# Performance work log

Measured on AMD Instinct MI355X. Metric: run time of the kernel, lower is better.

## Reference

```python
import jax, jax.numpy as jnp
import numpy as np

B, L, D, H, N = 1, 768, 128, 8, 6  # batch, seq len, model dim, heads, core_num
DH = D // H
EPS = 1e-5


def _layernorm(x, g, b):
    m = jnp.mean(x, axis=-1, keepdims=True)
    v = jnp.mean(jnp.square(x - m), axis=-1, keepdims=True)
    return (x - m) * jax.lax.rsqrt(v + EPS) * g + b


def setup_inputs() -> dict:
    key = jax.random.key(0)
    ks = jax.random.split(key, 12)
    s = 0.05

    def w(k, shape):
        return jax.random.normal(k, shape, dtype=jnp.float32) * s

    return {
        "x": jax.random.normal(ks[0], (B, L, D), dtype=jnp.float32),
        # JCrossOutProduct: l (in->mid), lo (mid->out); torch Linear convention y = x @ W.T + b
        "cop_l_w": w(ks[1], (N, D, D)), "cop_l_b": jnp.zeros((N, D), jnp.float32),
        "cop_lo_w": w(ks[2], (N, D, D)), "cop_lo_b": jnp.zeros((N, D), jnp.float32),
        # JResCOPAttn.l
        "cop_out_w": w(ks[3], (N, D, D)), "cop_out_b": jnp.zeros((N, D), jnp.float32),
        "cop_ln_g": jnp.ones((N, D), jnp.float32), "cop_ln_b": jnp.zeros((N, D), jnp.float32),
        # nn.MultiheadAttention: packed qkv in_proj + out_proj
        "qkv_w": w(ks[4], (N, 3 * D, D)), "qkv_b": jnp.zeros((N, 3 * D), jnp.float32),
        "mha_out_w": w(ks[5], (N, D, D)), "mha_out_b": jnp.zeros((N, D), jnp.float32),
        "mha_ln_g": jnp.ones((N, D), jnp.float32), "mha_ln_b": jnp.zeros((N, D), jnp.float32),
        # final l1
        "l1_w": w(ks[6], (D, D)), "l1_b": jnp.zeros((D,), jnp.float32),
    }


def reference(x, cop_l_w, cop_l_b, cop_lo_w, cop_lo_b, cop_out_w, cop_out_b,
              cop_ln_g, cop_ln_b, qkv_w, qkv_b, mha_out_w, mha_out_b,
              mha_ln_g, mha_ln_b, l1_w, l1_b):
    scale = 1.0 / np.sqrt(DH)
    for i in range(N):
        # ---- JResCOPAttn branch (AlphaFold-style outer product mean) ----
        a = x @ cop_l_w[i].T + cop_l_b[i]                          # [B,L,D]
        tm = jnp.einsum('bic,bjc->bijc', a, a)                     # [B,L,L,D] outer product
        tm = jnp.einsum('bijc,oc->bijo', tm, cop_lo_w[i]) + cop_lo_b[i]
        tx = x @ cop_out_w[i].T + cop_out_b[i]                     # [B,L,D]
        y1 = x + jnp.einsum('bijo,bjo->bio', tm, tx)               # '...cab,...ab->...cb'
        x1 = _layernorm(y1, cop_ln_g[i], cop_ln_b[i])              # dropout/act are identity
        # ---- JResSelfAttn branch (standard MHA, batch_first) ----
        qkv = x @ qkv_w[i].T + qkv_b[i]                            # [B,L,3D]
        q, k, v = jnp.split(qkv, 3, axis=-1)
        q = q.reshape(B, L, H, DH)
        k = k.reshape(B, L, H, DH)
        v = v.reshape(B, L, H, DH)
        scores = jnp.einsum('bihd,bjhd->bhij', q, k) * scale       # [B,H,L,L]
        attn = jax.nn.softmax(scores, axis=-1)
        o = jnp.einsum('bhij,bjhd->bihd', attn, v).reshape(B, L, D)
        y2 = x + (o @ mha_out_w[i].T + mha_out_b[i])
        x2 = _layernorm(y2, mha_ln_g[i], mha_ln_b[i])
        # ---- combine ----
        x = x + x1 + x2
    return x @ l1_w.T + l1_b
```

## Files before the change

kernel.cpp:

```cpp
#include <hip/hip_runtime.h>

#define L_SEQ 768
#define P_SZ  (L_SEQ * 128)

__device__ __forceinline__ void stage16(int tid, int r0, bool first,
    bool writeback, const float* xprev, const float* y1, const float* y2,
    const float* g1, const float* b1, const float* g2, const float* b2,
    float* xcur, float (*As)[132])
{
    const int row = tid >> 4;
    const int cs  = (tid & 15) * 8;
    const int gr  = (r0 + row) * 128 + cs;
    if (first) {
#pragma unroll
        for (int u = 0; u < 2; ++u)
            *(float4*)&As[row][cs + 4 * u] = *(const float4*)&xprev[gr + 4 * u];
        return;
    }
    float4 v1[2], v2[2];
    float s1 = 0.0f, s2 = 0.0f;
#pragma unroll
    for (int u = 0; u < 2; ++u) {
        v1[u] = *(const float4*)&y1[gr + 4 * u];
        v2[u] = *(const float4*)&y2[gr + 4 * u];
        s1 += v1[u].x + v1[u].y + v1[u].z + v1[u].w;
        s2 += v2[u].x + v2[u].y + v2[u].z + v2[u].w;
    }
#pragma unroll
    for (int m = 1; m < 16; m <<= 1) { s1 += __shfl_xor(s1, m); s2 += __shfl_xor(s2, m); }
    const float mu1 = s1 * (1.0f / 128.0f), mu2 = s2 * (1.0f / 128.0f);
    float q1 = 0.0f, q2 = 0.0f;
#pragma unroll
    for (int u = 0; u < 2; ++u) {
        float d;
        d = v1[u].x - mu1; q1 += d * d;  d = v1[u].y - mu1; q1 += d * d;
        d = v1[u].z - mu1; q1 += d * d;  d = v1[u].w - mu1; q1 += d * d;
        d = v2[u].x - mu2; q2 += d * d;  d = v2[u].y - mu2; q2 += d * d;
        d = v2[u].z - mu2; q2 += d * d;  d = v2[u].w - mu2; q2 += d * d;
    }
#pragma unroll
    for (int m = 1; m < 16; m <<= 1) { q1 += __shfl_xor(q1, m); q2 += __shfl_xor(q2, m); }
    const float rs1 = rsqrtf(q1 * (1.0f / 128.0f) + 1e-5f);
    const float rs2 = rsqrtf(q2 * (1.0f / 128.0f) + 1e-5f);
#pragma unroll
    for (int u = 0; u < 2; ++u) {
        float4 ga = *(const float4*)&g1[cs + 4 * u];
        float4 ba = *(const float4*)&b1[cs + 4 * u];
        float4 gb = *(const float4*)&g2[cs + 4 * u];
        float4 bb = *(const float4*)&b2[cs + 4 * u];
        float4 xv = *(const float4*)&xprev[gr + 4 * u];
        float4 o;
        o.x = xv.x + (v1[u].x - mu1) * rs1 * ga.x + ba.x + (v2[u].x - mu2) * rs2 * gb.x + bb.x;
        o.y = xv.y + (v1[u].y - mu1) * rs1 * ga.y + ba.y + (v2[u].y - mu2) * rs2 * gb.y + bb.y;
        o.z = xv.z + (v1[u].z - mu1) * rs1 * ga.z + ba.z + (v2[u].z - mu2) * rs2 * gb.z + bb.z;
        o.w = xv.w + (v1[u].w - mu1) * rs1 * ga.w + ba.w + (v2[u].w - mu2) * rs2 * gb.w + bb.w;
        *(float4*)&As[row][cs + 4 * u] = o;
        if (writeback) *(float4*)&xcur[gr + 4 * u] = o;
    }
}

__global__ __launch_bounds__(256, 4) void megaK(int first,
    const float* __restrict__ xprev, const float* __restrict__ y1,
    const float* __restrict__ y2, float* __restrict__ xcur,
    const float* __restrict__ g1, const float* __restrict__ b1,
    const float* __restrict__ g2, const float* __restrict__ b2,
    const float* __restrict__ lw, const float* __restrict__ lb,
    const float* __restrict__ ow, const float* __restrict__ ob,
    const float* __restrict__ qw, const float* __restrict__ qb,
    float* __restrict__ a, float* __restrict__ tx, float* __restrict__ qkv)
{
    __shared__ float Bs[64][132];
    __shared__ float As[16][132];
    const int bid = blockIdx.x;
    const int tid = threadIdx.x;
    const int ct = bid / 48, rt = bid % 48;
    const int r0 = rt * 16;
    stage16(tid, r0, first != 0, (!first && ct == 0), xprev, y1, y2,
            g1, b1, g2, b2, xcur, As);
    const float* W; const float* bias; float* outp; int ldC, colbase;
    if (ct < 2)      { W = lw; bias = lb; outp = a;   ldC = 128; colbase = ct * 64; }
    else if (ct < 4) { W = ow; bias = ob; outp = tx;  ldC = 128; colbase = (ct - 2) * 64; }
    else             { W = qw; bias = qb; outp = qkv; ldC = 384; colbase = (ct - 4) * 64; }
#pragma unroll
    for (int t = 0; t < 8; ++t) {
        int idx = tid + 256 * t;
        int brow = idx >> 5, f4 = idx & 31;
        *(float4*)&Bs[brow][f4 * 4] = *(const float4*)&W[(colbase + brow) * 128 + f4 * 4];
    }
    __syncthreads();
    const int rg = tid >> 4, ng = tid & 15;
    float accs[4];
#pragma unroll
    for (int c = 0; c < 4; ++c) accs[c] = bias[colbase + ng + 16 * c];
#pragma unroll 8
    for (int kk = 0; kk < 32; ++kk) {
        float4 a1 = *(const float4*)&As[rg][kk * 4];
#pragma unroll
        for (int c = 0; c < 4; ++c) {
            float4 b = *(const float4*)&Bs[ng + 16 * c][kk * 4];
            accs[c] += a1.x * b.x + a1.y * b.y + a1.z * b.z + a1.w * b.w;
        }
    }
    const int r = r0 + rg;
#pragma unroll
    for (int c = 0; c < 4; ++c)
        outp[r * ldC + colbase + ng + 16 * c] = accs[c];
}

__global__ __launch_bounds__(256, 4) void k2K(const float* __restrict__ qkv,
    const float* __restrict__ a_, const float* __restrict__ tx_,
    float* __restrict__ o_, float* __restrict__ Mpart, float* __restrict__ tspart)
{
    __shared__ __align__(16) char smem[49152];
    const int bid = blockIdx.x;
    const int tid = threadIdx.x;
    if (bid < 384) {
        float* Ks = (float*)smem;
        float* Vs = Ks + 192 * 20;
        float* sm = Vs + 192 * 20;
        float* sl = sm + 256;
        float* sacc = sl + 256;
        const int h = bid / 48;
        const int ch = bid % 48;
        const int r = tid & 15;
        const int part = tid >> 4;
        const int qi = ch * 16 + r;

        float q[16];
        {
            const float4* qr = (const float4*)(qkv + qi * 384 + h * 16);
#pragma unroll
            for (int s = 0; s < 4; ++s) {
                float4 v = qr[s];
                q[s * 4 + 0] = v.x; q[s * 4 + 1] = v.y;
                q[s * 4 + 2] = v.z; q[s * 4 + 3] = v.w;
            }
        }
        float m = -1e30f, l = 0.0f;
        float acc[16];
#pragma unroll
        for (int d = 0; d < 16; ++d) acc[d] = 0.0f;

        for (int s = 0; s < 4; ++s) {
            __syncthreads();
#pragma unroll
            for (int t = 0; t < 3; ++t) {
                int idx = tid + 256 * t;
                int row = idx >> 2, d4 = idx & 3;
                int j = s * 192 + row;
                *(float4*)&Ks[row * 20 + d4 * 4] =
                    *(const float4*)&qkv[j * 384 + 128 + h * 16 + d4 * 4];
                *(float4*)&Vs[row * 20 + d4 * 4] =
                    *(const float4*)&qkv[j * 384 + 256 + h * 16 + d4 * 4];
            }
            __syncthreads();
            const int tb = part * 12;
            for (int jj = 0; jj < 12; ++jj) {
                int t = tb + jj;
                float sc = 0.0f;
#pragma unroll
                for (int d = 0; d < 16; ++d) sc += q[d] * Ks[t * 20 + d];
                sc *= 0.25f;
                if (sc > m + 8.0f) {
                    float f = __expf(m - sc);
                    l *= f;
#pragma unroll
                    for (int d = 0; d < 16; ++d) acc[d] *= f;
                    m = sc;
                }
                float p = __expf(sc - m);
                l += p;
#pragma unroll
                for (int d = 0; d < 16; ++d) acc[d] += p * Vs[t * 20 + d];
            }
        }
        sm[part * 16 + r] = m;
        sl[part * 16 + r] = l;
#pragma unroll
        for (int d = 0; d < 16; ++d) sacc[(part * 16 + r) * 16 + d] = acc[d];
        __syncthreads();

        const int row = tid >> 4, d = tid & 15;
        float M = sm[row];
#pragma unroll
        for (int p = 1; p < 16; ++p) M = fmaxf(M, sm[p * 16 + row]);
        float L = 0.0f, o = 0.0f;
#pragma unroll
        for (int p = 0; p < 16; ++p) {
            float f = __expf(sm[p * 16 + row] - M);
            L += sl[p * 16 + row] * f;
            o += sacc[(p * 16 + row) * 16 + d] * f;
        }
        o_[(ch * 16 + row) * 128 + h * 16 + d] = o / L;
    } else {
        const int idx0 = bid - 384;
        const int jc = idx0 >> 2, ot = idx0 & 3;
        float* As  = (float*)smem;
        float* Ts  = As + 48 * 128;
        float* red = Ts + 48 * 32;
        const int c4 = tid & 31, owt = tid >> 5;
        float accm[4][4] = {};
        float tsacc = 0.0f;
        for (int half = 0; half < 2; ++half) {
            const int j0 = jc * 96 + half * 48;
            __syncthreads();
#pragma unroll
            for (int t = 0; t < 6; ++t) {
                int ix = tid + 256 * t;
                int jj = ix >> 5, f4 = ix & 31;
                *(float4*)&As[jj * 128 + f4 * 4] =
                    *(const float4*)&a_[(j0 + jj) * 128 + f4 * 4];
            }
#pragma unroll
            for (int t = 0; t < 2; ++t) {
                int ix = tid + 256 * t;
                if (ix < 384) {
                    int jj = ix >> 3, f4 = ix & 7;
                    *(float4*)&Ts[jj * 32 + f4 * 4] =
                        *(const float4*)&tx_[(j0 + jj) * 128 + ot * 32 + f4 * 4];
                }
            }
            __syncthreads();
#pragma unroll 4
            for (int jj = 0; jj < 48; ++jj) {
                float4 av = *(const float4*)&As[jj * 128 + c4 * 4];
                float4 tv = *(const float4*)&Ts[jj * 32 + owt * 4];
                float avv[4] = {av.x, av.y, av.z, av.w};
                float tvv[4] = {tv.x, tv.y, tv.z, tv.w};
#pragma unroll
                for (int oi = 0; oi < 4; ++oi)
#pragma unroll
                    for (int ci = 0; ci < 4; ++ci)
                        accm[oi][ci] += avv[ci] * tvv[oi];
            }
            {
                const int o = tid & 31, g = tid >> 5;
                float s = 0.0f;
#pragma unroll
                for (int jj = 0; jj < 6; ++jj) s += Ts[(g * 6 + jj) * 32 + o];
                tsacc += s;
            }
        }
#pragma unroll
        for (int oi = 0; oi < 4; ++oi) {
            *(float4*)&Mpart[jc * 16384 + (ot * 32 + owt * 4 + oi) * 128 + c4 * 4] =
                make_float4(accm[oi][0], accm[oi][1], accm[oi][2], accm[oi][3]);
        }
        __syncthreads();
        {
            const int o = tid & 31, g = tid >> 5;
            red[g * 32 + o] = tsacc;
        }
        __syncthreads();
        if (tid < 32) {
            float s = 0.0f;
#pragma unroll
            for (int g = 0; g < 8; ++g) s += red[g * 32 + tid];
            tspart[jc * 128 + ot * 32 + tid] = s;
        }
    }
}

__global__ __launch_bounds__(256, 4) void ygemmK(
    const float* __restrict__ a_, const float* __restrict__ o_,
    const float* __restrict__ Mpart, const float* __restrict__ lo_w,
    const float* __restrict__ lob, const float* __restrict__ tspart,
    const float* __restrict__ mw, const float* __restrict__ mb,
    const float* __restrict__ xc, float* __restrict__ y1, float* __restrict__ y2)
{
    __shared__ float Bs[64][132];
    const int bid = blockIdx.x;
    const int tid = threadIdx.x;
    const int yb = bid / 48, rt = bid % 48;
    const float* A; float* C; int colbase;
    if (yb < 2) {
        colbase = yb * 64; A = a_; C = y1;
#pragma unroll
        for (int t = 0; t < 8; ++t) {
            int idx = tid + 256 * t;
            int row = idx >> 5, f4 = idx & 31;
            int o = colbase + row;
            float4 s = make_float4(0.f, 0.f, 0.f, 0.f);
#pragma unroll
            for (int jc = 0; jc < 8; ++jc) {
                float4 mv = *(const float4*)&Mpart[jc * 16384 + o * 128 + f4 * 4];
                s.x += mv.x; s.y += mv.y; s.z += mv.z; s.w += mv.w;
            }
            float4 lw4 = *(const float4*)&lo_w[o * 128 + f4 * 4];
            s.x *= lw4.x; s.y *= lw4.y; s.z *= lw4.z; s.w *= lw4.w;
            *(float4*)&Bs[row][f4 * 4] = s;
        }
    } else {
        colbase = (yb - 2) * 64; A = o_; C = y2;
#pragma unroll
        for (int t = 0; t < 8; ++t) {
            int idx = tid + 256 * t;
            int row = idx >> 5, f4 = idx & 31;
            *(float4*)&Bs[row][f4 * 4] =
                *(const float4*)&mw[(colbase + row) * 128 + f4 * 4];
        }
    }
    __syncthreads();
    const int rg = tid >> 4, ng = tid & 15;
    const int r = rt * 16 + rg;
    float accs[4];
#pragma unroll
    for (int c = 0; c < 4; ++c) {
        int gc = colbase + ng + 16 * c;
        float bv;
        if (yb < 2) {
            float s = 0.0f;
#pragma unroll
            for (int jc = 0; jc < 8; ++jc) s += tspart[jc * 128 + gc];
            bv = lob[gc] * s;
        } else {
            bv = mb[gc];
        }
        accs[c] = bv;
    }
    const float* A1 = A + r * 128;
#pragma unroll 8
    for (int kk = 0; kk < 32; ++kk) {
        float4 a1 = *(const float4*)&A1[kk * 4];
#pragma unroll
        for (int c = 0; c < 4; ++c) {
            float4 b = *(const float4*)&Bs[ng + 16 * c][kk * 4];
            accs[c] += a1.x * b.x + a1.y * b.y + a1.z * b.z + a1.w * b.w;
        }
    }
#pragma unroll
    for (int c = 0; c < 4; ++c) {
        int gc = colbase + ng + 16 * c;
        C[r * 128 + gc] = xc[r * 128 + gc] + accs[c];
    }
}

__global__ __launch_bounds__(256, 4) void finK(
    const float* __restrict__ xprev, const float* __restrict__ y1,
    const float* __restrict__ y2,
    const float* __restrict__ g1, const float* __restrict__ b1,
    const float* __restrict__ g2, const float* __restrict__ b2,
    const float* __restrict__ w, const float* __restrict__ bias,
    float* __restrict__ outp)
{
    __shared__ float Bs[64][132];
    __shared__ float As[16][132];
    const int bid = blockIdx.x;
    const int tid = threadIdx.x;
    const int ct = bid / 48, rt = bid % 48;
    const int r0 = rt * 16;
    const int colbase = ct * 64;
    stage16(tid, r0, false, false, xprev, y1, y2, g1, b1, g2, b2, nullptr, As);
#pragma unroll
    for (int t = 0; t < 8; ++t) {
        int idx = tid + 256 * t;
        int brow = idx >> 5, f4 = idx & 31;
        *(float4*)&Bs[brow][f4 * 4] = *(const float4*)&w[(colbase + brow) * 128 + f4 * 4];
    }
    __syncthreads();
    const int rg = tid >> 4, ng = tid & 15;
    float accs[4];
#pragma unroll
    for (int c = 0; c < 4; ++c) accs[c] = bias[colbase + ng + 16 * c];
#pragma unroll 8
    for (int kk = 0; kk < 32; ++kk) {
        float4 a1 = *(const float4*)&As[rg][kk * 4];
#pragma unroll
        for (int c = 0; c < 4; ++c) {
            float4 b = *(const float4*)&Bs[ng + 16 * c][kk * 4];
            accs[c] += a1.x * b.x + a1.y * b.y + a1.z * b.z + a1.w * b.w;
        }
    }
    const int r = r0 + rg;
#pragma unroll
    for (int c = 0; c < 4; ++c)
        outp[r * 128 + colbase + ng + 16 * c] = accs[c];
}

extern "C" void kernel_launch(void* const* d_in, const int* in_sizes, int n_in,
                              void* d_out, int out_size, void* d_ws, size_t ws_size,
                              hipStream_t stream)
{
    const float* x_in      = (const float*)d_in[0];
    const float* cop_l_w   = (const float*)d_in[1];
    const float* cop_l_b   = (const float*)d_in[2];
    const float* cop_lo_w  = (const float*)d_in[3];
    const float* cop_lo_b  = (const float*)d_in[4];
    const float* cop_out_w = (const float*)d_in[5];
    const float* cop_out_b = (const float*)d_in[6];
    const float* cop_ln_g  = (const float*)d_in[7];
    const float* cop_ln_b  = (const float*)d_in[8];
    const float* qkv_w     = (const float*)d_in[9];
    const float* qkv_b     = (const float*)d_in[10];
    const float* mha_out_w = (const float*)d_in[11];
    const float* mha_out_b = (const float*)d_in[12];
    const float* mha_ln_g  = (const float*)d_in[13];
    const float* mha_ln_b  = (const float*)d_in[14];
    const float* l1_w      = (const float*)d_in[15];
    const float* l1_b      = (const float*)d_in[16];

    float* ws = (float*)d_ws;
    float* xA     = ws + 0 * P_SZ;
    float* xB     = ws + 1 * P_SZ;
    float* a_     = ws + 2 * P_SZ;
    float* tx_    = ws + 3 * P_SZ;
    float* y1_    = ws + 4 * P_SZ;
    float* y2_    = ws + 5 * P_SZ;
    float* qkv_   = ws + 6 * P_SZ;
    float* o_     = ws + 9 * P_SZ;
    float* Mpart  = ws + 10 * P_SZ;
    float* tspart = Mpart + 8 * 16384;

    const float* xc = x_in;

    for (int i = 0; i < 6; ++i) {
        const float* lw  = cop_l_w   + i * 16384;
        const float* lb  = cop_l_b   + i * 128;
        const float* low = cop_lo_w  + i * 16384;
        const float* lob = cop_lo_b  + i * 128;
        const float* ow  = cop_out_w + i * 16384;
        const float* ob  = cop_out_b + i * 128;
        const float* qw  = qkv_w     + i * 49152;
        const float* qb  = qkv_b     + i * 384;
        const float* mw  = mha_out_w + i * 16384;
        const float* mb  = mha_out_b + i * 128;
        const float* pg1 = cop_ln_g + (i - 1) * 128;
        const float* pb1 = cop_ln_b + (i - 1) * 128;
        const float* pg2 = mha_ln_g + (i - 1) * 128;
        const float* pb2 = mha_ln_b + (i - 1) * 128;

        if (i == 0) {
            megaK<<<480, 256, 0, stream>>>(1, x_in, nullptr, nullptr, nullptr,
                                           nullptr, nullptr, nullptr, nullptr,
                                           lw, lb, ow, ob, qw, qb, a_, tx_, qkv_);
        } else {
            float* xn = (i & 1) ? xB : xA;
            megaK<<<480, 256, 0, stream>>>(0, xc, y1_, y2_, xn,
                                           pg1, pb1, pg2, pb2,
                                           lw, lb, ow, ob, qw, qb, a_, tx_, qkv_);
            xc = xn;
        }
        k2K<<<416, 256, 0, stream>>>(qkv_, a_, tx_, o_, Mpart, tspart);
        ygemmK<<<192, 256, 0, stream>>>(a_, o_, Mpart, low, lob, tspart, mw, mb,
                                        xc, y1_, y2_);
    }

    finK<<<96, 256, 0, stream>>>(xc, y1_, y2_,
                                 cop_ln_g + 5 * 128, cop_ln_b + 5 * 128,
                                 mha_ln_g + 5 * 128, mha_ln_b + 5 * 128,
                                 l1_w, l1_b, (float*)d_out);
}
```

Baseline: 256.9 us.

## Fuse output projections into attention/COP kernel, drop ygemm kernel

```diff
diff --git a/kernel.cpp b/kernel.cpp
--- a/kernel.cpp
+++ b/kernel.cpp
@@ -67,7 +67,8 @@
     const float* __restrict__ lw, const float* __restrict__ lb,
     const float* __restrict__ ow, const float* __restrict__ ob,
     const float* __restrict__ qw, const float* __restrict__ qb,
-    float* __restrict__ a, float* __restrict__ tx, float* __restrict__ qkv)
+    float* __restrict__ a, float* __restrict__ tx, float* __restrict__ qkv,
+    float* __restrict__ y2i, const float* __restrict__ mbv)
 {
     __shared__ float Bs[64][132];
     __shared__ float As[16][132];
@@ -77,6 +78,18 @@
     const int r0 = rt * 16;
     stage16(tid, r0, first != 0, (!first && ct == 0), xprev, y1, y2,
             g1, b1, g2, b2, xcur, As);
+    if (ct == 0) {
+        const int row = tid >> 4, cs = (tid & 15) * 8;
+        const int gr = (r0 + row) * 128 + cs;
+        float4 m0 = *(const float4*)&mbv[cs];
+        float4 m1 = *(const float4*)&mbv[cs + 4];
+        float4 v0 = *(float4*)&As[row][cs];
+        float4 v1 = *(float4*)&As[row][cs + 4];
+        v0.x += m0.x; v0.y += m0.y; v0.z += m0.z; v0.w += m0.w;
+        v1.x += m1.x; v1.y += m1.y; v1.z += m1.z; v1.w += m1.w;
+        *(float4*)&y2i[gr] = v0;
+        *(float4*)&y2i[gr + 4] = v1;
+    }
     const float* W; const float* bias; float* outp; int ldC, colbase;
     if (ct < 2)      { W = lw; bias = lb; outp = a;   ldC = 128; colbase = ct * 64; }
     else if (ct < 4) { W = ow; bias = ob; outp = tx;  ldC = 128; colbase = (ct - 2) * 64; }
@@ -107,11 +120,13 @@
         outp[r * ldC + colbase + ng + 16 * c] = accs[c];
 }
 
-__global__ __launch_bounds__(256, 4) void k2K(const float* __restrict__ qkv,
+__global__ __launch_bounds__(256) void k2K(const float* __restrict__ qkv,
     const float* __restrict__ a_, const float* __restrict__ tx_,
-    float* __restrict__ o_, float* __restrict__ Mpart, float* __restrict__ tspart)
+    const float* __restrict__ xc, const float* __restrict__ lo_w,
+    const float* __restrict__ lob, const float* __restrict__ mw,
+    float* __restrict__ y1, float* __restrict__ y2)
 {
-    __shared__ __align__(16) char smem[49152];
+    __shared__ __align__(16) char smem[61440];
     const int bid = blockIdx.x;
     const int tid = threadIdx.x;
     if (bid < 384) {
@@ -180,158 +195,113 @@
         for (int d = 0; d < 16; ++d) sacc[(part * 16 + r) * 16 + d] = acc[d];
         __syncthreads();
 
-        const int row = tid >> 4, d = tid & 15;
-        float M = sm[row];
-#pragma unroll
-        for (int p = 1; p < 16; ++p) M = fmaxf(M, sm[p * 16 + row]);
-        float L = 0.0f, o = 0.0f;
-#pragma unroll
-        for (int p = 0; p < 16; ++p) {
-            float f = __expf(sm[p * 16 + row] - M);
-            L += sl[p * 16 + row] * f;
-            o += sacc[(p * 16 + row) * 16 + d] * f;
-        }
-        o_[(ch * 16 + row) * 128 + h * 16 + d] = o / L;
+        float* o16s = (float*)smem;
+        {
+            const int row = tid >> 4, d = tid & 15;
+            float M = sm[row];
+#pragma unroll
+            for (int p = 1; p < 16; ++p) M = fmaxf(M, sm[p * 16 + row]);
+            float L = 0.0f, o = 0.0f;
+#pragma unroll
+            for (int p = 0; p < 16; ++p) {
+                float f = __expf(sm[p * 16 + row] - M);
+                L += sl[p * 16 + row] * f;
+                o += sacc[(p * 16 + row) * 16 + d] * f;
+            }
+            o16s[row * 16 + d] = o / L;
+        }
+        __syncthreads();
+
+        {
+            const int r2 = tid >> 4, cg = tid & 15;
+            float ov[16];
+#pragma unroll
+            for (int s = 0; s < 4; ++s) {
+                float4 t = *(const float4*)&o16s[r2 * 16 + s * 4];
+                ov[s * 4 + 0] = t.x; ov[s * 4 + 1] = t.y;
+                ov[s * 4 + 2] = t.z; ov[s * 4 + 3] = t.w;
+            }
+            const int rg2 = ch * 16 + r2;
+#pragma unroll
+            for (int mm = 0; mm < 8; ++mm) {
+                int mcol = cg * 8 + mm;
+                const float* mwr = &mw[mcol * 128 + h * 16];
+                float s = 0.0f;
+#pragma unroll
+                for (int d2 = 0; d2 < 16; ++d2) s += ov[d2] * mwr[d2];
+                unsafeAtomicAdd(&y2[rg2 * 128 + mcol], s);
+            }
+        }
     } else {
-        const int idx0 = bid - 384;
-        const int jc = idx0 >> 2, ot = idx0 & 3;
+        const int oc0 = (bid - 384) * 8;
         float* As  = (float*)smem;
-        float* Ts  = As + 48 * 128;
-        float* red = Ts + 48 * 32;
-        const int c4 = tid & 31, owt = tid >> 5;
-        float accm[4][4] = {};
-        float tsacc = 0.0f;
-        for (int half = 0; half < 2; ++half) {
-            const int j0 = jc * 96 + half * 48;
-            __syncthreads();
-#pragma unroll
-            for (int t = 0; t < 6; ++t) {
+        float* Ts  = As + 96 * 132;
+        float* W2s = Ts + 96 * 8;
+        float* tss = W2s + 8 * 132;
+        const int c = tid & 127, oq = tid >> 7;
+        float macc[4] = {0.f, 0.f, 0.f, 0.f};
+        float tsl = 0.0f;
+        for (int jc = 0; jc < 8; ++jc) {
+            __syncthreads();
+#pragma unroll
+            for (int t = 0; t < 12; ++t) {
                 int ix = tid + 256 * t;
                 int jj = ix >> 5, f4 = ix & 31;
-                *(float4*)&As[jj * 128 + f4 * 4] =
-                    *(const float4*)&a_[(j0 + jj) * 128 + f4 * 4];
-            }
-#pragma unroll
-            for (int t = 0; t < 2; ++t) {
+                *(float4*)&As[jj * 132 + f4 * 4] =
+                    *(const float4*)&a_[(jc * 96 + jj) * 128 + f4 * 4];
+            }
+            if (tid < 192) {
+                int jj = tid >> 1, qq = tid & 1;
+                *(float4*)&Ts[jj * 8 + qq * 4] =
+                    *(const float4*)&tx_[(jc * 96 + jj) * 128 + oc0 + qq * 4];
+            }
+            __syncthreads();
+#pragma unroll 4
+            for (int jj = 0; jj < 96; ++jj) {
+                float av = As[jj * 132 + c];
+                float4 t4 = *(const float4*)&Ts[jj * 8 + oq * 4];
+                macc[0] += av * t4.x; macc[1] += av * t4.y;
+                macc[2] += av * t4.z; macc[3] += av * t4.w;
+            }
+            if (tid < 8) {
+                float s = 0.0f;
+                for (int jj = 0; jj < 96; ++jj) s += Ts[jj * 8 + tid];
+                tsl += s;
+            }
+        }
+        __syncthreads();
+#pragma unroll
+        for (int k = 0; k < 4; ++k) {
+            int o = oq * 4 + k;
+            W2s[o * 132 + c] = lo_w[(oc0 + o) * 128 + c] * macc[k];
+        }
+        if (tid < 8) tss[tid] = tsl;
+        __syncthreads();
+        for (int jc = 0; jc < 8; ++jc) {
+#pragma unroll
+            for (int t = 0; t < 12; ++t) {
                 int ix = tid + 256 * t;
-                if (ix < 384) {
-                    int jj = ix >> 3, f4 = ix & 7;
-                    *(float4*)&Ts[jj * 32 + f4 * 4] =
-                        *(const float4*)&tx_[(j0 + jj) * 128 + ot * 32 + f4 * 4];
+                int jj = ix >> 5, f4 = ix & 31;
+                *(float4*)&As[jj * 132 + f4 * 4] =
+                    *(const float4*)&a_[(jc * 96 + jj) * 128 + f4 * 4];
+            }
+            __syncthreads();
+#pragma unroll
+            for (int rep = 0; rep < 3; ++rep) {
+                int idx = tid + 256 * rep;
+                int jj = idx >> 3, o = idx & 7;
+                float s = 0.0f;
+#pragma unroll 8
+                for (int c4 = 0; c4 < 32; ++c4) {
+                    float4 av = *(const float4*)&As[jj * 132 + c4 * 4];
+                    float4 wv = *(const float4*)&W2s[o * 132 + c4 * 4];
+                    s += av.x * wv.x + av.y * wv.y + av.z * wv.z + av.w * wv.w;
                 }
-            }
-            __syncthreads();
-#pragma unroll 4
-            for (int jj = 0; jj < 48; ++jj) {
-                float4 av = *(const float4*)&As[jj * 128 + c4 * 4];
-                float4 tv = *(const float4*)&Ts[jj * 32 + owt * 4];
-                float avv[4] = {av.x, av.y, av.z, av.w};
-                float tvv[4] = {tv.x, tv.y, tv.z, tv.w};
-#pragma unroll
-                for (int oi = 0; oi < 4; ++oi)
-#pragma unroll
-                    for (int ci = 0; ci < 4; ++ci)
-                        accm[oi][ci] += avv[ci] * tvv[oi];
-            }
-            {
-                const int o = tid & 31, g = tid >> 5;
-                float s = 0.0f;
-#pragma unroll
-                for (int jj = 0; jj < 6; ++jj) s += Ts[(g * 6 + jj) * 32 + o];
-                tsacc += s;
-            }
-        }
-#pragma unroll
-        for (int oi = 0; oi < 4; ++oi) {
-            *(float4*)&Mpart[jc * 16384 + (ot * 32 + owt * 4 + oi) * 128 + c4 * 4] =
-                make_float4(accm[oi][0], accm[oi][1], accm[oi][2], accm[oi][3]);
-        }
-        __syncthreads();
-        {
-            const int o = tid & 31, g = tid >> 5;
-            red[g * 32 + o] = tsacc;
-        }
-        __syncthreads();
-        if (tid < 32) {
-            float s = 0.0f;
-#pragma unroll
-            for (int g = 0; g < 8; ++g) s += red[g * 32 + tid];
-            tspart[jc * 128 + ot * 32 + tid] = s;
-        }
-    }
-}
-
-__global__ __launch_bounds__(256, 4) void ygemmK(
-    const float* __restrict__ a_, const float* __restrict__ o_,
-    const float* __restrict__ Mpart, const float* __restrict__ lo_w,
-    const float* __restrict__ lob, const float* __restrict__ tspart,
-    const float* __restrict__ mw, const float* __restrict__ mb,
-    const float* __restrict__ xc, float* __restrict__ y1, float* __restrict__ y2)
-{
-    __shared__ float Bs[64][132];
-    const int bid = blockIdx.x;
-    const int tid = threadIdx.x;
-    const int yb = bid / 48, rt = bid % 48;
-    const float* A; float* C; int colbase;
-    if (yb < 2) {
-        colbase = yb * 64; A = a_; C = y1;
-#pragma unroll
-        for (int t = 0; t < 8; ++t) {
-            int idx = tid + 256 * t;
-            int row = idx >> 5, f4 = idx & 31;
-            int o = colbase + row;
-            float4 s = make_float4(0.f, 0.f, 0.f, 0.f);
-#pragma unroll
-            for (int jc = 0; jc < 8; ++jc) {
-                float4 mv = *(const float4*)&Mpart[jc * 16384 + o * 128 + f4 * 4];
-                s.x += mv.x; s.y += mv.y; s.z += mv.z; s.w += mv.w;
-            }
-            float4 lw4 = *(const float4*)&lo_w[o * 128 + f4 * 4];
-            s.x *= lw4.x; s.y *= lw4.y; s.z *= lw4.z; s.w *= lw4.w;
-            *(float4*)&Bs[row][f4 * 4] = s;
-        }
-    } else {
-        colbase = (yb - 2) * 64; A = o_; C = y2;
-#pragma unroll
-        for (int t = 0; t < 8; ++t) {
-            int idx = tid + 256 * t;
-            int row = idx >> 5, f4 = idx & 31;
-            *(float4*)&Bs[row][f4 * 4] =
-                *(const float4*)&mw[(colbase + row) * 128 + f4 * 4];
-        }
-    }
-    __syncthreads();
-    const int rg = tid >> 4, ng = tid & 15;
-    const int r = rt * 16 + rg;
-    float accs[4];
-#pragma unroll
-    for (int c = 0; c < 4; ++c) {
-        int gc = colbase + ng + 16 * c;
-        float bv;
-        if (yb < 2) {
-            float s = 0.0f;
-#pragma unroll
-            for (int jc = 0; jc < 8; ++jc) s += tspart[jc * 128 + gc];
-            bv = lob[gc] * s;
-        } else {
-            bv = mb[gc];
-        }
-        accs[c] = bv;
-    }
-    const float* A1 = A + r * 128;
-#pragma unroll 8
-    for (int kk = 0; kk < 32; ++kk) {
-        float4 a1 = *(const float4*)&A1[kk * 4];
-#pragma unroll
-        for (int c = 0; c < 4; ++c) {
-            float4 b = *(const float4*)&Bs[ng + 16 * c][kk * 4];
-            accs[c] += a1.x * b.x + a1.y * b.y + a1.z * b.z + a1.w * b.w;
-        }
-    }
-#pragma unroll
-    for (int c = 0; c < 4; ++c) {
-        int gc = colbase + ng + 16 * c;
-        C[r * 128 + gc] = xc[r * 128 + gc] + accs[c];
+                int gj = jc * 96 + jj, go = oc0 + o;
+                y1[gj * 128 + go] = xc[gj * 128 + go] + s + lob[go] * tss[o];
+            }
+            __syncthreads();
+        }
     }
 }
 
@@ -400,16 +370,14 @@
     const float* l1_b      = (const float*)d_in[16];
 
     float* ws = (float*)d_ws;
-    float* xA     = ws + 0 * P_SZ;
-    float* xB     = ws + 1 * P_SZ;
-    float* a_     = ws + 2 * P_SZ;
-    float* tx_    = ws + 3 * P_SZ;
-    float* y1_    = ws + 4 * P_SZ;
-    float* y2_    = ws + 5 * P_SZ;
-    float* qkv_   = ws + 6 * P_SZ;
-    float* o_     = ws + 9 * P_SZ;
-    float* Mpart  = ws + 10 * P_SZ;
-    float* tspart = Mpart + 8 * 16384;
+    float* xA   = ws + 0 * P_SZ;
+    float* xB   = ws + 1 * P_SZ;
+    float* a_   = ws + 2 * P_SZ;
+    float* tx_  = ws + 3 * P_SZ;
+    float* y1_  = ws + 4 * P_SZ;
+    float* y2A  = ws + 5 * P_SZ;
+    float* y2B  = ws + 6 * P_SZ;
+    float* qkv_ = ws + 7 * P_SZ;
 
     const float* xc = x_in;
 
@@ -429,23 +397,26 @@
         const float* pg2 = mha_ln_g + (i - 1) * 128;
         const float* pb2 = mha_ln_b + (i - 1) * 128;
 
+        float* y2cur  = (i & 1) ? y2B : y2A;
+        float* y2prev = (i & 1) ? y2A : y2B;
+
         if (i == 0) {
             megaK<<<480, 256, 0, stream>>>(1, x_in, nullptr, nullptr, nullptr,
                                            nullptr, nullptr, nullptr, nullptr,
-                                           lw, lb, ow, ob, qw, qb, a_, tx_, qkv_);
+                                           lw, lb, ow, ob, qw, qb, a_, tx_, qkv_,
+                                           y2cur, mb);
         } else {
             float* xn = (i & 1) ? xB : xA;
-            megaK<<<480, 256, 0, stream>>>(0, xc, y1_, y2_, xn,
+            megaK<<<480, 256, 0, stream>>>(0, xc, y1_, y2prev, xn,
                                            pg1, pb1, pg2, pb2,
-                                           lw, lb, ow, ob, qw, qb, a_, tx_, qkv_);
+                                           lw, lb, ow, ob, qw, qb, a_, tx_, qkv_,
+                                           y2cur, mb);
             xc = xn;
         }
-        k2K<<<416, 256, 0, stream>>>(qkv_, a_, tx_, o_, Mpart, tspart);
-        ygemmK<<<192, 256, 0, stream>>>(a_, o_, Mpart, low, lob, tspart, mw, mb,
-                                        xc, y1_, y2_);
-    }
-
-    finK<<<96, 256, 0, stream>>>(xc, y1_, y2_,
+        k2K<<<400, 256, 0, stream>>>(qkv_, a_, tx_, xc, low, lob, mw, y1_, y2cur);
+    }
+
+    finK<<<96, 256, 0, stream>>>(xc, y1_, y2B,
                                  cop_ln_g + 5 * 128, cop_ln_b + 5 * 128,
                                  mha_ln_g + 5 * 128, mha_ln_b + 5 * 128,
                                  l1_w, l1_b, (float*)d_out);
```

Result: slower. 487.3 us (+89.7%).

## Stage all K rows in LDS once and stream V directly from global memory

Applied to the files above, without the earlier changes.

```diff
diff --git a/kernel.cpp b/kernel.cpp
--- a/kernel.cpp
+++ b/kernel.cpp
@@ -107,19 +107,15 @@
         outp[r * ldC + colbase + ng + 16 * c] = accs[c];
 }
 
-__global__ __launch_bounds__(256, 4) void k2K(const float* __restrict__ qkv,
+__global__ __launch_bounds__(256, 3) void k2K(const float* __restrict__ qkv,
     const float* __restrict__ a_, const float* __restrict__ tx_,
     float* __restrict__ o_, float* __restrict__ Mpart, float* __restrict__ tspart)
 {
-    __shared__ __align__(16) char smem[49152];
+    __shared__ __align__(16) char smem[50176];
     const int bid = blockIdx.x;
     const int tid = threadIdx.x;
     if (bid < 384) {
         float* Ks = (float*)smem;
-        float* Vs = Ks + 192 * 20;
-        float* sm = Vs + 192 * 20;
-        float* sl = sm + 256;
-        float* sacc = sl + 256;
         const int h = bid / 48;
         const int ch = bid % 48;
         const int r = tid & 15;
@@ -136,44 +132,58 @@
                 q[s * 4 + 2] = v.z; q[s * 4 + 3] = v.w;
             }
         }
+#pragma unroll
+        for (int t = 0; t < 12; ++t) {
+            int idx = tid + 256 * t;
+            int row = idx >> 2, seg = idx & 3;
+            *(float4*)&Ks[row * 16 + (row / 48) * 4 + seg * 4] =
+                *(const float4*)&qkv[row * 384 + 128 + h * 16 + seg * 4];
+        }
+        __syncthreads();
+
         float m = -1e30f, l = 0.0f;
         float acc[16];
 #pragma unroll
         for (int d = 0; d < 16; ++d) acc[d] = 0.0f;
 
-        for (int s = 0; s < 4; ++s) {
-            __syncthreads();
-#pragma unroll
-            for (int t = 0; t < 3; ++t) {
-                int idx = tid + 256 * t;
-                int row = idx >> 2, d4 = idx & 3;
-                int j = s * 192 + row;
-                *(float4*)&Ks[row * 20 + d4 * 4] =
-                    *(const float4*)&qkv[j * 384 + 128 + h * 16 + d4 * 4];
-                *(float4*)&Vs[row * 20 + d4 * 4] =
-                    *(const float4*)&qkv[j * 384 + 256 + h * 16 + d4 * 4];
-            }
-            __syncthreads();
-            const int tb = part * 12;
-            for (int jj = 0; jj < 12; ++jj) {
-                int t = tb + jj;
-                float sc = 0.0f;
-#pragma unroll
-                for (int d = 0; d < 16; ++d) sc += q[d] * Ks[t * 20 + d];
-                sc *= 0.25f;
-                if (sc > m + 8.0f) {
-                    float f = __expf(m - sc);
-                    l *= f;
-#pragma unroll
-                    for (int d = 0; d < 16; ++d) acc[d] *= f;
-                    m = sc;
-                }
-                float p = __expf(sc - m);
-                l += p;
-#pragma unroll
-                for (int d = 0; d < 16; ++d) acc[d] += p * Vs[t * 20 + d];
-            }
-        }
+        const int tb = part * 48;
+        const int kb = part * 772;
+        const float* vcol = qkv + 256 + h * 16;
+#pragma unroll 2
+        for (int jj = 0; jj < 48; ++jj) {
+            const float* vr = vcol + (tb + jj) * 384;
+            float4 va = *(const float4*)vr;
+            float4 vb = *(const float4*)(vr + 4);
+            float4 vc = *(const float4*)(vr + 8);
+            float4 vd = *(const float4*)(vr + 12);
+            const float* kr = &Ks[kb + jj * 16];
+            float sc = 0.0f;
+#pragma unroll
+            for (int s = 0; s < 4; ++s) {
+                float4 k4 = *(const float4*)(kr + s * 4);
+                sc += q[s * 4 + 0] * k4.x + q[s * 4 + 1] * k4.y +
+                      q[s * 4 + 2] * k4.z + q[s * 4 + 3] * k4.w;
+            }
+            sc *= 0.25f;
+            if (sc > m + 8.0f) {
+                float f = __expf(m - sc);
+                l *= f;
+#pragma unroll
+                for (int d = 0; d < 16; ++d) acc[d] *= f;
+                m = sc;
+            }
+            float p = __expf(sc - m);
+            l += p;
+            acc[0]  += p * va.x; acc[1]  += p * va.y; acc[2]  += p * va.z; acc[3]  += p * va.w;
+            acc[4]  += p * vb.x; acc[5]  += p * vb.y; acc[6]  += p * vb.z; acc[7]  += p * vb.w;
+            acc[8]  += p * vc.x; acc[9]  += p * vc.y; acc[10] += p * vc.z; acc[11] += p * vc.w;
+            acc[12] += p * vd.x; acc[13] += p * vd.y; acc[14] += p * vd.z; acc[15] += p * vd.w;
+        }
+        __syncthreads();
+
+        float* sm = (float*)smem;
+        float* sl = sm + 256;
+        float* sacc = sl + 256;
         sm[part * 16 + r] = m;
         sl[part * 16 + r] = l;
 #pragma unroll
```

Result: slower. 266.7 us (+3.8%).

## Fuse y-GEMMs into next megakernel and reduce COP partials with atomics

Applied to the files above, without the earlier changes.

```diff
diff --git a/kernel.cpp b/kernel.cpp
--- a/kernel.cpp
+++ b/kernel.cpp
@@ -3,98 +3,128 @@
 #define L_SEQ 768
 #define P_SZ  (L_SEQ * 128)
 
-__device__ __forceinline__ void stage16(int tid, int r0, bool first,
-    bool writeback, const float* xprev, const float* y1, const float* y2,
-    const float* g1, const float* b1, const float* g2, const float* b2,
-    float* xcur, float (*As)[132])
-{
-    const int row = tid >> 4;
-    const int cs  = (tid & 15) * 8;
-    const int gr  = (r0 + row) * 128 + cs;
-    if (first) {
-#pragma unroll
-        for (int u = 0; u < 2; ++u)
-            *(float4*)&As[row][cs + 4 * u] = *(const float4*)&xprev[gr + 4 * u];
-        return;
-    }
-    float4 v1[2], v2[2];
-    float s1 = 0.0f, s2 = 0.0f;
-#pragma unroll
-    for (int u = 0; u < 2; ++u) {
-        v1[u] = *(const float4*)&y1[gr + 4 * u];
-        v2[u] = *(const float4*)&y2[gr + 4 * u];
-        s1 += v1[u].x + v1[u].y + v1[u].z + v1[u].w;
-        s2 += v2[u].x + v2[u].y + v2[u].z + v2[u].w;
-    }
-#pragma unroll
-    for (int m = 1; m < 16; m <<= 1) { s1 += __shfl_xor(s1, m); s2 += __shfl_xor(s2, m); }
-    const float mu1 = s1 * (1.0f / 128.0f), mu2 = s2 * (1.0f / 128.0f);
-    float q1 = 0.0f, q2 = 0.0f;
-#pragma unroll
-    for (int u = 0; u < 2; ++u) {
-        float d;
-        d = v1[u].x - mu1; q1 += d * d;  d = v1[u].y - mu1; q1 += d * d;
-        d = v1[u].z - mu1; q1 += d * d;  d = v1[u].w - mu1; q1 += d * d;
-        d = v2[u].x - mu2; q2 += d * d;  d = v2[u].y - mu2; q2 += d * d;
-        d = v2[u].z - mu2; q2 += d * d;  d = v2[u].w - mu2; q2 += d * d;
-    }
-#pragma unroll
-    for (int m = 1; m < 16; m <<= 1) { q1 += __shfl_xor(q1, m); q2 += __shfl_xor(q2, m); }
-    const float rs1 = rsqrtf(q1 * (1.0f / 128.0f) + 1e-5f);
-    const float rs2 = rsqrtf(q2 * (1.0f / 128.0f) + 1e-5f);
-#pragma unroll
-    for (int u = 0; u < 2; ++u) {
-        float4 ga = *(const float4*)&g1[cs + 4 * u];
-        float4 ba = *(const float4*)&b1[cs + 4 * u];
-        float4 gb = *(const float4*)&g2[cs + 4 * u];
-        float4 bb = *(const float4*)&b2[cs + 4 * u];
-        float4 xv = *(const float4*)&xprev[gr + 4 * u];
-        float4 o;
-        o.x = xv.x + (v1[u].x - mu1) * rs1 * ga.x + ba.x + (v2[u].x - mu2) * rs2 * gb.x + bb.x;
-        o.y = xv.y + (v1[u].y - mu1) * rs1 * ga.y + ba.y + (v2[u].y - mu2) * rs2 * gb.y + bb.y;
-        o.z = xv.z + (v1[u].z - mu1) * rs1 * ga.z + ba.z + (v2[u].z - mu2) * rs2 * gb.z + bb.z;
-        o.w = xv.w + (v1[u].w - mu1) * rs1 * ga.w + ba.w + (v2[u].w - mu2) * rs2 * gb.w + bb.w;
-        *(float4*)&As[row][cs + 4 * u] = o;
-        if (writeback) *(float4*)&xcur[gr + 4 * u] = o;
-    }
-}
-
-__global__ __launch_bounds__(256, 4) void megaK(int first,
-    const float* __restrict__ xprev, const float* __restrict__ y1,
-    const float* __restrict__ y2, float* __restrict__ xcur,
+__global__ __launch_bounds__(256, 3) void megaK(int first,
+    const float* __restrict__ xprev, float* __restrict__ xcur,
+    const float* __restrict__ aPrev, const float* __restrict__ oPrev,
+    const float* __restrict__ W2rd, const float* __restrict__ tsrd,
+    float* __restrict__ W2zero, float* __restrict__ tszero,
+    const float* __restrict__ lobP, const float* __restrict__ mwP,
+    const float* __restrict__ mbP,
     const float* __restrict__ g1, const float* __restrict__ b1,
     const float* __restrict__ g2, const float* __restrict__ b2,
     const float* __restrict__ lw, const float* __restrict__ lb,
     const float* __restrict__ ow, const float* __restrict__ ob,
     const float* __restrict__ qw, const float* __restrict__ qb,
-    float* __restrict__ a, float* __restrict__ tx, float* __restrict__ qkv)
+    float* __restrict__ aOut, float* __restrict__ tx, float* __restrict__ qkv)
 {
     __shared__ float Bs[64][132];
-    __shared__ float As[16][132];
+    __shared__ float Ap[16][132];
+    __shared__ float OpAs[16][132];
     const int bid = blockIdx.x;
     const int tid = threadIdx.x;
     const int ct = bid / 48, rt = bid % 48;
     const int r0 = rt * 16;
-    stage16(tid, r0, first != 0, (!first && ct == 0), xprev, y1, y2,
-            g1, b1, g2, b2, xcur, As);
+
+    if (bid < 128) {
+        if (tid < 32)
+            *(float4*)&W2zero[bid * 128 + tid * 4] = make_float4(0.f, 0.f, 0.f, 0.f);
+    } else if (bid == 128) {
+        if (tid < 32)
+            *(float4*)&tszero[tid * 4] = make_float4(0.f, 0.f, 0.f, 0.f);
+    }
+
     const float* W; const float* bias; float* outp; int ldC, colbase;
-    if (ct < 2)      { W = lw; bias = lb; outp = a;   ldC = 128; colbase = ct * 64; }
-    else if (ct < 4) { W = ow; bias = ob; outp = tx;  ldC = 128; colbase = (ct - 2) * 64; }
-    else             { W = qw; bias = qb; outp = qkv; ldC = 384; colbase = (ct - 4) * 64; }
+    if (ct < 2)      { W = lw; bias = lb; outp = aOut; ldC = 128; colbase = ct * 64; }
+    else if (ct < 4) { W = ow; bias = ob; outp = tx;   ldC = 128; colbase = (ct - 2) * 64; }
+    else             { W = qw; bias = qb; outp = qkv;  ldC = 384; colbase = (ct - 4) * 64; }
 #pragma unroll
     for (int t = 0; t < 8; ++t) {
         int idx = tid + 256 * t;
         int brow = idx >> 5, f4 = idx & 31;
         *(float4*)&Bs[brow][f4 * 4] = *(const float4*)&W[(colbase + brow) * 128 + f4 * 4];
     }
-    __syncthreads();
+
+    const int row = tid >> 4;
+    const int cs  = (tid & 15) * 8;
+    const int gr  = (r0 + row) * 128 + cs;
+
+    if (first) {
+        *(float4*)&OpAs[row][cs]     = *(const float4*)&xprev[gr];
+        *(float4*)&OpAs[row][cs + 4] = *(const float4*)&xprev[gr + 4];
+        __syncthreads();
+    } else {
+#pragma unroll
+        for (int t = 0; t < 2; ++t) {
+            int idx = tid + 256 * t;
+            int rr = idx >> 5, f4 = idx & 31;
+            *(float4*)&Ap[rr][f4 * 4]   = *(const float4*)&aPrev[(r0 + rr) * 128 + f4 * 4];
+            *(float4*)&OpAs[rr][f4 * 4] = *(const float4*)&oPrev[(r0 + rr) * 128 + f4 * 4];
+        }
+        __syncthreads();
+
+        float y1v[8], y2v[8];
+#pragma unroll
+        for (int cc = 0; cc < 8; ++cc) { y1v[cc] = 0.f; y2v[cc] = 0.f; }
+        for (int k4 = 0; k4 < 32; ++k4) {
+            float4 av = *(const float4*)&Ap[row][k4 * 4];
+            float4 ov = *(const float4*)&OpAs[row][k4 * 4];
+#pragma unroll
+            for (int cc = 0; cc < 8; ++cc) {
+                int c = cs + cc;
+                float4 wv = *(const float4*)&W2rd[c * 128 + k4 * 4];
+                float4 mv = *(const float4*)&mwP[c * 128 + k4 * 4];
+                y1v[cc] += av.x * wv.x + av.y * wv.y + av.z * wv.z + av.w * wv.w;
+                y2v[cc] += ov.x * mv.x + ov.y * mv.y + ov.z * mv.z + ov.w * mv.w;
+            }
+        }
+        float4 xv0 = *(const float4*)&xprev[gr];
+        float4 xv1 = *(const float4*)&xprev[gr + 4];
+        float xvv[8] = {xv0.x, xv0.y, xv0.z, xv0.w, xv1.x, xv1.y, xv1.z, xv1.w};
+        float s1 = 0.f, s2 = 0.f;
+#pragma unroll
+        for (int cc = 0; cc < 8; ++cc) {
+            int c = cs + cc;
+            y1v[cc] += xvv[cc] + lobP[c] * tsrd[c];
+            y2v[cc] += xvv[cc] + mbP[c];
+            s1 += y1v[cc]; s2 += y2v[cc];
+        }
+#pragma unroll
+        for (int mm = 1; mm < 16; mm <<= 1) { s1 += __shfl_xor(s1, mm); s2 += __shfl_xor(s2, mm); }
+        const float mu1 = s1 * (1.0f / 128.0f), mu2 = s2 * (1.0f / 128.0f);
+        float q1 = 0.f, q2 = 0.f;
+#pragma unroll
+        for (int cc = 0; cc < 8; ++cc) {
+            float d1 = y1v[cc] - mu1; q1 += d1 * d1;
+            float d2 = y2v[cc] - mu2; q2 += d2 * d2;
+        }
+#pragma unroll
+        for (int mm = 1; mm < 16; mm <<= 1) { q1 += __shfl_xor(q1, mm); q2 += __shfl_xor(q2, mm); }
+        const float rs1 = rsqrtf(q1 * (1.0f / 128.0f) + 1e-5f);
+        const float rs2 = rsqrtf(q2 * (1.0f / 128.0f) + 1e-5f);
+        float res[8];
+#pragma unroll
+        for (int cc = 0; cc < 8; ++cc) {
+            int c = cs + cc;
+            res[cc] = xvv[cc] + (y1v[cc] - mu1) * rs1 * g1[c] + b1[c]
+                              + (y2v[cc] - mu2) * rs2 * g2[c] + b2[c];
+        }
+        __syncthreads();
+        *(float4*)&OpAs[row][cs]     = make_float4(res[0], res[1], res[2], res[3]);
+        *(float4*)&OpAs[row][cs + 4] = make_float4(res[4], res[5], res[6], res[7]);
+        if (ct == 0) {
+            *(float4*)&xcur[gr]     = make_float4(res[0], res[1], res[2], res[3]);
+            *(float4*)&xcur[gr + 4] = make_float4(res[4], res[5], res[6], res[7]);
+        }
+        __syncthreads();
+    }
+
     const int rg = tid >> 4, ng = tid & 15;
     float accs[4];
 #pragma unroll
     for (int c = 0; c < 4; ++c) accs[c] = bias[colbase + ng + 16 * c];
 #pragma unroll 8
     for (int kk = 0; kk < 32; ++kk) {
-        float4 a1 = *(const float4*)&As[rg][kk * 4];
+        float4 a1 = *(const float4*)&OpAs[rg][kk * 4];
 #pragma unroll
         for (int c = 0; c < 4; ++c) {
             float4 b = *(const float4*)&Bs[ng + 16 * c][kk * 4];
@@ -109,7 +139,8 @@
 
 __global__ __launch_bounds__(256, 4) void k2K(const float* __restrict__ qkv,
     const float* __restrict__ a_, const float* __restrict__ tx_,
-    float* __restrict__ o_, float* __restrict__ Mpart, float* __restrict__ tspart)
+    float* __restrict__ o_, float* __restrict__ W2acc, float* __restrict__ tsg,
+    const float* __restrict__ lo_w)
 {
     __shared__ __align__(16) char smem[49152];
     const int bid = blockIdx.x;
@@ -200,7 +231,7 @@
         float* red = Ts + 48 * 32;
         const int c4 = tid & 31, owt = tid >> 5;
         float accm[4][4] = {};
-        float tsacc = 0.0f;
+        float tsl = 0.0f;
         for (int half = 0; half < 2; ++half) {
             const int j0 = jc * 96 + half * 48;
             __syncthreads();
@@ -238,133 +269,128 @@
                 float s = 0.0f;
 #pragma unroll
                 for (int jj = 0; jj < 6; ++jj) s += Ts[(g * 6 + jj) * 32 + o];
-                tsacc += s;
+                tsl += s;
             }
         }
 #pragma unroll
         for (int oi = 0; oi < 4; ++oi) {
-            *(float4*)&Mpart[jc * 16384 + (ot * 32 + owt * 4 + oi) * 128 + c4 * 4] =
-                make_float4(accm[oi][0], accm[oi][1], accm[oi][2], accm[oi][3]);
+            int o = ot * 32 + owt * 4 + oi;
+            const float* lwr = &lo_w[o * 128 + c4 * 4];
+            float* w2r = &W2acc[o * 128 + c4 * 4];
+            unsafeAtomicAdd(&w2r[0], lwr[0] * accm[oi][0]);
+            unsafeAtomicAdd(&w2r[1], lwr[1] * accm[oi][1]);
+            unsafeAtomicAdd(&w2r[2], lwr[2] * accm[oi][2]);
+            unsafeAtomicAdd(&w2r[3], lwr[3] * accm[oi][3]);
         }
         __syncthreads();
         {
             const int o = tid & 31, g = tid >> 5;
-            red[g * 32 + o] = tsacc;
+            red[g * 32 + o] = tsl;
         }
         __syncthreads();
         if (tid < 32) {
             float s = 0.0f;
 #pragma unroll
             for (int g = 0; g < 8; ++g) s += red[g * 32 + tid];
-            tspart[jc * 128 + ot * 32 + tid] = s;
+            unsafeAtomicAdd(&tsg[ot * 32 + tid], s);
         }
     }
 }
 
-__global__ __launch_bounds__(256, 4) void ygemmK(
-    const float* __restrict__ a_, const float* __restrict__ o_,
-    const float* __restrict__ Mpart, const float* __restrict__ lo_w,
-    const float* __restrict__ lob, const float* __restrict__ tspart,
-    const float* __restrict__ mw, const float* __restrict__ mb,
-    const float* __restrict__ xc, float* __restrict__ y1, float* __restrict__ y2)
-{
-    __shared__ float Bs[64][132];
-    const int bid = blockIdx.x;
-    const int tid = threadIdx.x;
-    const int yb = bid / 48, rt = bid % 48;
-    const float* A; float* C; int colbase;
-    if (yb < 2) {
-        colbase = yb * 64; A = a_; C = y1;
-#pragma unroll
-        for (int t = 0; t < 8; ++t) {
-            int idx = tid + 256 * t;
-            int row = idx >> 5, f4 = idx & 31;
-            int o = colbase + row;
-            float4 s = make_float4(0.f, 0.f, 0.f, 0.f);
-#pragma unroll
-            for (int jc = 0; jc < 8; ++jc) {
-                float4 mv = *(const float4*)&Mpart[jc * 16384 + o * 128 + f4 * 4];
-                s.x += mv.x; s.y += mv.y; s.z += mv.z; s.w += mv.w;
-            }
-            float4 lw4 = *(const float4*)&lo_w[o * 128 + f4 * 4];
-            s.x *= lw4.x; s.y *= lw4.y; s.z *= lw4.z; s.w *= lw4.w;
-            *(float4*)&Bs[row][f4 * 4] = s;
-        }
-    } else {
-        colbase = (yb - 2) * 64; A = o_; C = y2;
-#pragma unroll
-        for (int t = 0; t < 8; ++t) {
-            int idx = tid + 256 * t;
-            int row = idx >> 5, f4 = idx & 31;
-            *(float4*)&Bs[row][f4 * 4] =
-                *(const float4*)&mw[(colbase + row) * 128 + f4 * 4];
-        }
-    }
-    __syncthreads();
-    const int rg = tid >> 4, ng = tid & 15;
-    const int r = rt * 16 + rg;
-    float accs[4];
-#pragma unroll
-    for (int c = 0; c < 4; ++c) {
-        int gc = colbase + ng + 16 * c;
-        float bv;
-        if (yb < 2) {
-            float s = 0.0f;
-#pragma unroll
-            for (int jc = 0; jc < 8; ++jc) s += tspart[jc * 128 + gc];
-            bv = lob[gc] * s;
-        } else {
-            bv = mb[gc];
-        }
-        accs[c] = bv;
-    }
-    const float* A1 = A + r * 128;
-#pragma unroll 8
-    for (int kk = 0; kk < 32; ++kk) {
-        float4 a1 = *(const float4*)&A1[kk * 4];
-#pragma unroll
-        for (int c = 0; c < 4; ++c) {
-            float4 b = *(const float4*)&Bs[ng + 16 * c][kk * 4];
-            accs[c] += a1.x * b.x + a1.y * b.y + a1.z * b.z + a1.w * b.w;
-        }
-    }
-#pragma unroll
-    for (int c = 0; c < 4; ++c) {
-        int gc = colbase + ng + 16 * c;
-        C[r * 128 + gc] = xc[r * 128 + gc] + accs[c];
-    }
-}
-
-__global__ __launch_bounds__(256, 4) void finK(
-    const float* __restrict__ xprev, const float* __restrict__ y1,
-    const float* __restrict__ y2,
+__global__ __launch_bounds__(256, 3) void finK(
+    const float* __restrict__ xprev,
+    const float* __restrict__ aPrev, const float* __restrict__ oPrev,
+    const float* __restrict__ W2rd, const float* __restrict__ tsrd,
+    const float* __restrict__ lobP, const float* __restrict__ mwP,
+    const float* __restrict__ mbP,
     const float* __restrict__ g1, const float* __restrict__ b1,
     const float* __restrict__ g2, const float* __restrict__ b2,
     const float* __restrict__ w, const float* __restrict__ bias,
     float* __restrict__ outp)
 {
     __shared__ float Bs[64][132];
-    __shared__ float As[16][132];
+    __shared__ float Ap[16][132];
+    __shared__ float OpAs[16][132];
     const int bid = blockIdx.x;
     const int tid = threadIdx.x;
     const int ct = bid / 48, rt = bid % 48;
     const int r0 = rt * 16;
     const int colbase = ct * 64;
-    stage16(tid, r0, false, false, xprev, y1, y2, g1, b1, g2, b2, nullptr, As);
 #pragma unroll
     for (int t = 0; t < 8; ++t) {
         int idx = tid + 256 * t;
         int brow = idx >> 5, f4 = idx & 31;
         *(float4*)&Bs[brow][f4 * 4] = *(const float4*)&w[(colbase + brow) * 128 + f4 * 4];
     }
+    const int row = tid >> 4;
+    const int cs  = (tid & 15) * 8;
+    const int gr  = (r0 + row) * 128 + cs;
+#pragma unroll
+    for (int t = 0; t < 2; ++t) {
+        int idx = tid + 256 * t;
+        int rr = idx >> 5, f4 = idx & 31;
+        *(float4*)&Ap[rr][f4 * 4]   = *(const float4*)&aPrev[(r0 + rr) * 128 + f4 * 4];
+        *(float4*)&OpAs[rr][f4 * 4] = *(const float4*)&oPrev[(r0 + rr) * 128 + f4 * 4];
+    }
     __syncthreads();
+    float y1v[8], y2v[8];
+#pragma unroll
+    for (int cc = 0; cc < 8; ++cc) { y1v[cc] = 0.f; y2v[cc] = 0.f; }
+    for (int k4 = 0; k4 < 32; ++k4) {
+        float4 av = *(const float4*)&Ap[row][k4 * 4];
+        float4 ov = *(const float4*)&OpAs[row][k4 * 4];
+#pragma unroll
+        for (int cc = 0; cc < 8; ++cc) {
+            int c = cs + cc;
+            float4 wv = *(const float4*)&W2rd[c * 128 + k4 * 4];
+            float4 mv = *(const float4*)&mwP[c * 128 + k4 * 4];
+            y1v[cc] += av.x * wv.x + av.y * wv.y + av.z * wv.z + av.w * wv.w;
+            y2v[cc] += ov.x * mv.x + ov.y * mv.y + ov.z * mv.z + ov.w * mv.w;
+        }
+    }
+    float4 xv0 = *(const float4*)&xprev[gr];
+    float4 xv1 = *(const float4*)&xprev[gr + 4];
+    float xvv[8] = {xv0.x, xv0.y, xv0.z, xv0.w, xv1.x, xv1.y, xv1.z, xv1.w};
+    float s1 = 0.f, s2 = 0.f;
+#pragma unroll
+    for (int cc = 0; cc < 8; ++cc) {
+        int c = cs + cc;
+        y1v[cc] += xvv[cc] + lobP[c] * tsrd[c];
+        y2v[cc] += xvv[cc] + mbP[c];
+        s1 += y1v[cc]; s2 += y2v[cc];
+    }
+#pragma unroll
+    for (int mm = 1; mm < 16; mm <<= 1) { s1 += __shfl_xor(s1, mm); s2 += __shfl_xor(s2, mm); }
+    const float mu1 = s1 * (1.0f / 128.0f), mu2 = s2 * (1.0f / 128.0f);
+    float q1 = 0.f, q2 = 0.f;
+#pragma unroll
+    for (int cc = 0; cc < 8; ++cc) {
+        float d1 = y1v[cc] - mu1; q1 += d1 * d1;
+        float d2 = y2v[cc] - mu2; q2 += d2 * d2;
+    }
+#pragma unroll
+    for (int mm = 1; mm < 16; mm <<= 1) { q1 += __shfl_xor(q1, mm); q2 += __shfl_xor(q2, mm); }
+    const float rs1 = rsqrtf(q1 * (1.0f / 128.0f) + 1e-5f);
+    const float rs2 = rsqrtf(q2 * (1.0f / 128.0f) + 1e-5f);
+    float res[8];
+#pragma unroll
+    for (int cc = 0; cc < 8; ++cc) {
+        int c = cs + cc;
+        res[cc] = xvv[cc] + (y1v[cc] - mu1) * rs1 * g1[c] + b1[c]
+                          + (y2v[cc] - mu2) * rs2 * g2[c] + b2[c];
+    }
+    __syncthreads();
+    *(float4*)&OpAs[row][cs]     = make_float4(res[0], res[1], res[2], res[3]);
+    *(float4*)&OpAs[row][cs + 4] = make_float4(res[4], res[5], res[6], res[7]);
+    __syncthreads();
+
     const int rg = tid >> 4, ng = tid & 15;
     float accs[4];
 #pragma unroll
     for (int c = 0; c < 4; ++c) accs[c] = bias[colbase + ng + 16 * c];
 #pragma unroll 8
     for (int kk = 0; kk < 32; ++kk) {
-        float4 a1 = *(const float4*)&As[rg][kk * 4];
+        float4 a1 = *(const float4*)&OpAs[rg][kk * 4];
 #pragma unroll
         for (int c = 0; c < 4; ++c) {
             float4 b = *(const float4*)&Bs[ng + 16 * c][kk * 4];
@@ -400,16 +426,17 @@
     const float* l1_b      = (const float*)d_in[16];
 
     float* ws = (float*)d_ws;
-    float* xA     = ws + 0 * P_SZ;
-    float* xB     = ws + 1 * P_SZ;
-    float* a_     = ws + 2 * P_SZ;
-    float* tx_    = ws + 3 * P_SZ;
-    float* y1_    = ws + 4 * P_SZ;
-    float* y2_    = ws + 5 * P_SZ;
-    float* qkv_   = ws + 6 * P_SZ;
-    float* o_     = ws + 9 * P_SZ;
-    float* Mpart  = ws + 10 * P_SZ;
-    float* tspart = Mpart + 8 * 16384;
+    float* xA   = ws + 0 * P_SZ;
+    float* xB   = ws + 1 * P_SZ;
+    float* aA   = ws + 2 * P_SZ;
+    float* aB   = ws + 3 * P_SZ;
+    float* tx_  = ws + 4 * P_SZ;
+    float* qkv_ = ws + 5 * P_SZ;
+    float* o_   = ws + 8 * P_SZ;
+    float* W2A  = ws + 9 * P_SZ;
+    float* W2B  = W2A + 16384;
+    float* tsA  = W2B + 16384;
+    float* tsB  = tsA + 128;
 
     const float* xc = x_in;
 
@@ -417,35 +444,47 @@
         const float* lw  = cop_l_w   + i * 16384;
         const float* lb  = cop_l_b   + i * 128;
         const float* low = cop_lo_w  + i * 16384;
-        const float* lob = cop_lo_b  + i * 128;
         const float* ow  = cop_out_w + i * 16384;
         const float* ob  = cop_out_b + i * 128;
         const float* qw  = qkv_w     + i * 49152;
         const float* qb  = qkv_b     + i * 384;
-        const float* mw  = mha_out_w + i * 16384;
-        const float* mb  = mha_out_b + i * 128;
-        const float* pg1 = cop_ln_g + (i - 1) * 128;
-        const float* pb1 = cop_ln_b + (i - 1) * 128;
-        const float* pg2 = mha_ln_g + (i - 1) * 128;
-        const float* pb2 = mha_ln_b + (i - 1) * 128;
+
+        float* aCur = (i & 1) ? aB : aA;
+        const float* aPrv = (i & 1) ? aA : aB;
+        float* W2cur = (i & 1) ? W2B : W2A;
+        const float* W2prv = (i & 1) ? W2A : W2B;
+        float* tscur = (i & 1) ? tsB : tsA;
+        const float* tsprv = (i & 1) ? tsA : tsB;
 
         if (i == 0) {
             megaK<<<480, 256, 0, stream>>>(1, x_in, nullptr, nullptr, nullptr,
+                                           nullptr, nullptr, W2cur, tscur,
+                                           nullptr, nullptr, nullptr,
                                            nullptr, nullptr, nullptr, nullptr,
-                                           lw, lb, ow, ob, qw, qb, a_, tx_, qkv_);
+                                           lw, lb, ow, ob, qw, qb,
+                                           aCur, tx_, qkv_);
         } else {
             float* xn = (i & 1) ? xB : xA;
-            megaK<<<480, 256, 0, stream>>>(0, xc, y1_, y2_, xn,
-                                           pg1, pb1, pg2, pb2,
-                                           lw, lb, ow, ob, qw, qb, a_, tx_, qkv_);
+            megaK<<<480, 256, 0, stream>>>(0, xc, xn, aPrv, o_,
+                                           W2prv, tsprv, W2cur, tscur,
+                                           cop_lo_b + (i - 1) * 128,
+                                           mha_out_w + (i - 1) * 16384,
+                                           mha_out_b + (i - 1) * 128,
+                                           cop_ln_g + (i - 1) * 128,
+                                           cop_ln_b + (i - 1) * 128,
+                                           mha_ln_g + (i - 1) * 128,
+                                           mha_ln_b + (i - 1) * 128,
+                                           lw, lb, ow, ob, qw, qb,
+                                           aCur, tx_, qkv_);
             xc = xn;
         }
-        k2K<<<416, 256, 0, stream>>>(qkv_, a_, tx_, o_, Mpart, tspart);
-        ygemmK<<<192, 256, 0, stream>>>(a_, o_, Mpart, low, lob, tspart, mw, mb,
-                                        xc, y1_, y2_);
-    }
-
-    finK<<<96, 256, 0, stream>>>(xc, y1_, y2_,
+        k2K<<<416, 256, 0, stream>>>(qkv_, aCur, tx_, o_, W2cur, tscur, low);
+    }
+
+    finK<<<96, 256, 0, stream>>>(xc, aB, o_, W2B, tsB,
+                                 cop_lo_b + 5 * 128,
+                                 mha_out_w + 5 * 16384,
+                                 mha_out_b + 5 * 128,
                                  cop_ln_g + 5 * 128, cop_ln_b + 5 * 128,
                                  mha_ln_g + 5 * 128, mha_ln_b + 5 * 128,
                                  l1_w, l1_b, (float*)d_out);
```

Result: slower. 769.8 us (+199.7%).
